# Kernel optimization log

Hardware: AMD Instinct MI355X
Metric: run time of the kernel (lower is better)

The kernel has to match this reference:

```python
import jax, jax.numpy as jnp
import numpy as np

N = 100000

def _gcn_layer(x, W, b, src, dst, norm):
    # dense transform then sparse normalized aggregation (scatter-add)
    h = x @ W                                  # [N, out]
    msg = h[src] * norm[:, None]               # [E+N, out]
    agg = jax.ops.segment_sum(msg, dst, num_segments=N)
    return agg + b


def setup_inputs() -> dict:
    key = jax.random.key(0)
    ks = jax.random.split(key, 12)
    num_features, hidden, num_classes = 128, 128, 32
    E = 3200000
    x = jax.random.normal(ks[0], (N, num_features), dtype=jnp.float32)
    edge_index = jax.random.randint(ks[1], (2, E), 0, N, dtype=jnp.int64)

    def glorot(k, fan_in, fan_out):
        s = (6.0 / (fan_in + fan_out)) ** 0.5
        return jax.random.uniform(k, (fan_in, fan_out), jnp.float32, -s, s)

    return {
        "x": x,
        "edge_index": edge_index,
        "W1": glorot(ks[2], num_features, hidden), "b1": jnp.zeros((hidden,), jnp.float32),
        "W2": glorot(ks[3], hidden, hidden),       "b2": jnp.zeros((hidden,), jnp.float32),
        "W3": glorot(ks[4], hidden, hidden),       "b3": jnp.zeros((hidden,), jnp.float32),
        "W4": glorot(ks[5], hidden, num_classes),  "b4": jnp.zeros((num_classes,), jnp.float32),
    }


def reference(x, edge_index, W1, b1, W2, b2, W3, b3, W4, b4):
    # GCNConv semantics: add self-loops, symmetric degree normalization
    loop = jnp.arange(N, dtype=edge_index.dtype)
    src = jnp.concatenate([edge_index[0], loop])   # [E+N]
    dst = jnp.concatenate([edge_index[1], loop])   # [E+N]
    deg = jax.ops.segment_sum(jnp.ones_like(dst, dtype=x.dtype), dst, num_segments=N)
    dinv = jnp.where(deg > 0, deg ** -0.5, 0.0)
    norm = dinv[src] * dinv[dst]                   # [E+N]

    h = _gcn_layer(x, W1, b1, src, dst, norm)
    h = jax.nn.relu(h)                              # dropout: eval mode -> identity
    h = _gcn_layer(h, W2, b2, src, dst, norm)
    h = jax.nn.relu(h)
    h = _gcn_layer(h, W3, b3, src, dst, norm)
    h = jax.nn.relu(h)
    h = _gcn_layer(h, W4, b4, src, dst, norm)
    return jax.nn.log_softmax(h, axis=1)
```

## Files before the change

### kernel.cpp

```cpp
#include <hip/hip_runtime.h>
#include <hip/hip_bf16.h>
#include <math.h>

#define NNODES 100000
#define NBMAX 512
#define CH 8192

typedef __hip_bfloat16 bf16;
typedef __attribute__((ext_vector_type(8))) short short8;
typedef __attribute__((ext_vector_type(4))) float f32x4;
typedef __attribute__((ext_vector_type(2))) float f32x2;

__device__ inline unsigned pack_bf16x2(float a, float b) {
    __hip_bfloat162 p;
    p.x = __float2bfloat16(a);
    p.y = __float2bfloat16(b);
    return *(unsigned*)&p;
}

__device__ inline float2 unpack_bf16x2(unsigned u) {
    __hip_bfloat162 p = *(__hip_bfloat162*)&u;
    return make_float2(__bfloat162float(p.x), __bfloat162float(p.y));
}

__device__ inline unsigned char f32_to_fp8(float v) {
    int p = __builtin_amdgcn_cvt_pk_fp8_f32(v, v, 0, false);
    return (unsigned char)(p & 0xff);
}

__global__ __launch_bounds__(256) void prep_w_all(const float* __restrict__ W1, bf16* __restrict__ wt1,
                                                  const float* __restrict__ W2, bf16* __restrict__ wt2,
                                                  const float* __restrict__ W3, bf16* __restrict__ wt3,
                                                  const float* __restrict__ W4, bf16* __restrict__ wt4,
                                                  int* __restrict__ bcount, int* __restrict__ done,
                                                  unsigned* __restrict__ zrow) {
    int b = blockIdx.x, t = threadIdx.x;
    if (b == 0) {
        for (int i = t; i < NBMAX; i += 256) bcount[i] = 0;
        if (t == 0) *done = 0;
        if (t < 32) zrow[t] = 0u;
    }
    const float* W; bf16* WT; int Nout, idx0;
    if (b < 64)       { W = W1; WT = wt1; Nout = 128; idx0 = b * 256; }
    else if (b < 128) { W = W2; WT = wt2; Nout = 128; idx0 = (b - 64) * 256; }
    else if (b < 192) { W = W3; WT = wt3; Nout = 128; idx0 = (b - 128) * 256; }
    else              { W = W4; WT = wt4; Nout = 32;  idx0 = (b - 192) * 256; }
    int idx = idx0 + t;
    if (idx < 128 * Nout) {
        int nn = idx >> 7;
        int kk = idx & 127;
        WT[idx] = __float2bfloat16(W[kk * Nout + nn]);
    }
}

__global__ __launch_bounds__(256) void bucket_hist_scan(const int* __restrict__ dst,
                                                        int* __restrict__ bcount,
                                                        int* __restrict__ boff,
                                                        int* __restrict__ bcursor,
                                                        int* __restrict__ done,
                                                        int E, int nb, int nblocks) {
    __shared__ int hist[NBMAX];
    __shared__ int ticket_s;
    __shared__ int wsum[4];
    int t = threadIdx.x;
    for (int i = t; i < NBMAX; i += 256) hist[i] = 0;
    __syncthreads();
    int e0 = blockIdx.x * CH;
#pragma unroll
    for (int k = 0; k < 32; ++k) {
        int e = e0 + t + k * 256;
        if (e < E) atomicAdd(&hist[dst[e] >> 8], 1);
    }
    __syncthreads();
    for (int i = t; i < nb; i += 256)
        if (hist[i]) atomicAdd(&bcount[i], hist[i]);
    __threadfence();
    __syncthreads();
    if (t == 0) ticket_s = atomicAdd(done, 1);
    __syncthreads();
    if (ticket_s != nblocks - 1) return;
    __threadfence();
    int i0 = t * 2, i1v = t * 2 + 1;
    int a  = (i0  < nb) ? atomicAdd(&bcount[i0], 0) : 0;
    int bb = (i1v < nb) ? atomicAdd(&bcount[i1v], 0) : 0;
    int v = a + bb;
    int lane = t & 63, wv = t >> 6;
    int incl = v;
#pragma unroll
    for (int dd = 1; dd < 64; dd <<= 1) {
        int x = __shfl_up(incl, dd, 64);
        if (lane >= dd) incl += x;
    }
    if (lane == 63) wsum[wv] = incl;
    __syncthreads();
    int wo = 0;
    for (int k = 0; k < wv; ++k) wo += wsum[k];
    int excl = wo + incl - v;
    if (i0 <= nb)  { boff[i0]  = excl;     if (i0  < nb) bcursor[i0]  = excl; }
    if (i1v <= nb) { boff[i1v] = excl + a; if (i1v < nb) bcursor[i1v] = excl + a; }
}

__global__ __launch_bounds__(256) void partition(const int* __restrict__ src,
                                                 const int* __restrict__ dst,
                                                 int* __restrict__ bcursor,
                                                 int* __restrict__ part, int E, int nb) {
    __shared__ int hist[NBMAX];
    __shared__ int cursor[NBMAX];
    int t = threadIdx.x;
    int e0 = blockIdx.x * CH;
    for (int i = t; i < NBMAX; i += 256) hist[i] = 0;
    __syncthreads();
    int mys[32], myd[32];
#pragma unroll
    for (int k = 0; k < 32; ++k) {
        int e = e0 + t + k * 256;
        int s = 0, dd = -1;
        if (e < E) { s = src[e]; dd = dst[e]; }
        mys[k] = s; myd[k] = dd;
        if (dd >= 0) atomicAdd(&hist[dd >> 8], 1);
    }
    __syncthreads();
    for (int i = t; i < nb; i += 256) {
        int c = hist[i];
        cursor[i] = c ? atomicAdd(&bcursor[i], c) : 0;
    }
    __syncthreads();
#pragma unroll
    for (int k = 0; k < 32; ++k) {
        int dd = myd[k];
        if (dd >= 0) {
            int lpos = atomicAdd(&cursor[dd >> 8], 1);
            part[lpos] = mys[k] | ((dd & 255) << 24);
        }
    }
}

__global__ __launch_bounds__(256) void nodes_fill(const int* __restrict__ part,
                                                  const int* __restrict__ boff,
                                                  float* __restrict__ dinv,
                                                  int2* __restrict__ off2,
                                                  int* __restrict__ edges, int n) {
    __shared__ int ndeg[256];
    __shared__ int ws2[4];
    __shared__ int offl[256];
    int b = blockIdx.x;
    int t = threadIdx.x;
    ndeg[t] = 0;
    __syncthreads();
    int r0 = boff[b], r1 = boff[b + 1];
    for (int i = r0 + t; i < r1; i += 256)
        atomicAdd(&ndeg[((unsigned)part[i]) >> 24], 1);
    __syncthreads();
    int deg = ndeg[t];
    int node = b * 256 + t;
    int lane = t & 63, wv = t >> 6;
    int incl = deg;
#pragma unroll
    for (int d = 1; d < 64; d <<= 1) {
        int x = __shfl_up(incl, d, 64);
        if (lane >= d) incl += x;
    }
    if (lane == 63) ws2[wv] = incl;
    __syncthreads();
    int wo = 0;
    for (int k = 0; k < wv; ++k) wo += ws2[k];
    int node_off = r0 + wo + incl - deg;
    if (node < n) {
        off2[node] = make_int2(node_off, node_off + deg);
        dinv[node] = rsqrtf((float)(deg + 1));
    }
    offl[t] = node_off;
    ndeg[t] = 0;
    __syncthreads();
    for (int i = r0 + t; i < r1; i += 256) {
        int rec = part[i];
        int dloc = ((unsigned)rec) >> 24;
        int lpos = atomicAdd(&ndeg[dloc], 1);
        edges[offl[dloc] + lpos] = rec & 0xFFFFFF;
    }
}

#define WSTRIDE 136

__global__ __launch_bounds__(256) void gemm128_f32A(const float* __restrict__ A,
                                                    const bf16* __restrict__ WT,
                                                    const float* __restrict__ dinv,
                                                    unsigned char* __restrict__ C, int n) {
    __shared__ bf16 wl[128 * WSTRIDE];
    int t = threadIdx.x;
#pragma unroll
    for (int l = 0; l < 8; ++l) {
        int chunk = t + l * 256;
        int row = chunk >> 4, ch = chunk & 15;
        *(uint4*)&wl[row * WSTRIDE + ch * 8] = *(const uint4*)&WT[row * 128 + ch * 8];
    }
    __syncthreads();
    int wave = t >> 6, lane = t & 63;
    int m = lane & 15, q = lane >> 4;
    int row_base = blockIdx.x * 128 + wave * 32;
    int r0 = min(row_base + m, n - 1);
    int r1 = min(row_base + 16 + m, n - 1);

    f32x4 acc[2][8];
#pragma unroll
    for (int g = 0; g < 2; ++g)
#pragma unroll
        for (int c = 0; c < 8; ++c) acc[g][c] = (f32x4)(0.f);

#pragma unroll
    for (int kt = 0; kt < 4; ++kt) {
        short8 af[2];
#pragma unroll
        for (int g = 0; g < 2; ++g) {
            const float* ap = &A[(size_t)(g ? r1 : r0) * 128 + kt * 32 + q * 8];
            float4 f0 = *(const float4*)ap;
            float4 f1 = *(const float4*)(ap + 4);
            union { uint4 u; short8 s; } cv;
            cv.u.x = pack_bf16x2(f0.x, f0.y);
            cv.u.y = pack_bf16x2(f0.z, f0.w);
            cv.u.z = pack_bf16x2(f1.x, f1.y);
            cv.u.w = pack_bf16x2(f1.z, f1.w);
            af[g] = cv.s;
        }
#pragma unroll
        for (int c = 0; c < 8; ++c) {
            short8 bf = *(const short8*)&wl[(c * 16 + m) * WSTRIDE + kt * 32 + q * 8];
            acc[0][c] = __builtin_amdgcn_mfma_f32_16x16x32_bf16(af[0], bf, acc[0][c], 0, 0, 0);
            acc[1][c] = __builtin_amdgcn_mfma_f32_16x16x32_bf16(af[1], bf, acc[1][c], 0, 0, 0);
        }
    }
    float dv[2][4];
#pragma unroll
    for (int g = 0; g < 2; ++g)
#pragma unroll
        for (int r = 0; r < 4; ++r) {
            int row = row_base + g * 16 + q * 4 + r;
            dv[g][r] = (row < n) ? dinv[row] : 0.f;
        }
#pragma unroll
    for (int g = 0; g < 2; ++g)
#pragma unroll
        for (int c = 0; c < 8; ++c)
#pragma unroll
            for (int r = 0; r < 4; ++r) {
                int row = row_base + g * 16 + q * 4 + r;
                if (row < n) C[(size_t)row * 128 + c * 16 + m] = f32_to_fp8(acc[g][c][r] * dv[g][r]);
            }
}

__global__ __launch_bounds__(256) void gemm128_bf16A(const bf16* __restrict__ A,
                                                     const bf16* __restrict__ WT,
                                                     const float* __restrict__ dinv,
                                                     unsigned char* __restrict__ C, int n) {
    __shared__ bf16 wl[128 * WSTRIDE];
    int t = threadIdx.x;
#pragma unroll
    for (int l = 0; l < 8; ++l) {
        int chunk = t + l * 256;
        int row = chunk >> 4, ch = chunk & 15;
        *(uint4*)&wl[row * WSTRIDE + ch * 8] = *(const uint4*)&WT[row * 128 + ch * 8];
    }
    __syncthreads();
    int wave = t >> 6, lane = t & 63;
    int m = lane & 15, q = lane >> 4;
    int row_base = blockIdx.x * 128 + wave * 32;
    int r0 = min(row_base + m, n - 1);
    int r1 = min(row_base + 16 + m, n - 1);

    f32x4 acc[2][8];
#pragma unroll
    for (int g = 0; g < 2; ++g)
#pragma unroll
        for (int c = 0; c < 8; ++c) acc[g][c] = (f32x4)(0.f);

#pragma unroll
    for (int kt = 0; kt < 4; ++kt) {
        short8 a0 = *(const short8*)&A[(size_t)r0 * 128 + kt * 32 + q * 8];
        short8 a1 = *(const short8*)&A[(size_t)r1 * 128 + kt * 32 + q * 8];
#pragma unroll
        for (int c = 0; c < 8; ++c) {
            short8 bf = *(const short8*)&wl[(c * 16 + m) * WSTRIDE + kt * 32 + q * 8];
            acc[0][c] = __builtin_amdgcn_mfma_f32_16x16x32_bf16(a0, bf, acc[0][c], 0, 0, 0);
            acc[1][c] = __builtin_amdgcn_mfma_f32_16x16x32_bf16(a1, bf, acc[1][c], 0, 0, 0);
        }
    }
    float dv[2][4];
#pragma unroll
    for (int g = 0; g < 2; ++g)
#pragma unroll
        for (int r = 0; r < 4; ++r) {
            int row = row_base + g * 16 + q * 4 + r;
            dv[g][r] = (row < n) ? dinv[row] : 0.f;
        }
#pragma unroll
    for (int g = 0; g < 2; ++g)
#pragma unroll
        for (int c = 0; c < 8; ++c)
#pragma unroll
            for (int r = 0; r < 4; ++r) {
                int row = row_base + g * 16 + q * 4 + r;
                if (row < n) C[(size_t)row * 128 + c * 16 + m] = f32_to_fp8(acc[g][c][r] * dv[g][r]);
            }
}

__global__ __launch_bounds__(256) void gemm32_bf16A(const bf16* __restrict__ A,
                                                    const bf16* __restrict__ WT,
                                                    const float* __restrict__ dinv,
                                                    bf16* __restrict__ C, int n) {
    if (blockIdx.x == 0 && threadIdx.x < 32)
        C[(size_t)n * 32 + threadIdx.x] = __float2bfloat16(0.f);
    int wave = threadIdx.x >> 6;
    int lane = threadIdx.x & 63;
    int m = lane & 15;
    int q = lane >> 4;
    int row_base = blockIdx.x * 64 + wave * 16;
    int arow = min(row_base + m, n - 1);

    f32x4 acc[2];
    acc[0] = (f32x4)(0.f);
    acc[1] = (f32x4)(0.f);

#pragma unroll
    for (int kt = 0; kt < 4; ++kt) {
        short8 af = *(const short8*)&A[(size_t)arow * 128 + kt * 32 + q * 8];
#pragma unroll
        for (int c = 0; c < 2; ++c) {
            short8 bf = *(const short8*)&WT[(size_t)(c * 16 + m) * 128 + kt * 32 + q * 8];
            acc[c] = __builtin_amdgcn_mfma_f32_16x16x32_bf16(af, bf, acc[c], 0, 0, 0);
        }
    }
    float dv[4];
#pragma unroll
    for (int r = 0; r < 4; ++r) {
        int row = row_base + q * 4 + r;
        dv[r] = (row < n) ? dinv[row] : 0.f;
    }
#pragma unroll
    for (int c = 0; c < 2; ++c)
#pragma unroll
        for (int r = 0; r < 4; ++r) {
            int row = row_base + q * 4 + r;
            if (row < n) C[(size_t)row * 32 + c * 16 + m] = __float2bfloat16(acc[c][r] * dv[r]);
        }
}

__global__ __launch_bounds__(256) void agg128(const unsigned char* __restrict__ h,
                                              const int2* __restrict__ off2,
                                              const int* __restrict__ edges,
                                              const float* __restrict__ dinv,
                                              const float* __restrict__ bias,
                                              bf16* __restrict__ out, int n) {
    int wid = (blockIdx.x * blockDim.x + threadIdx.x) >> 6;
    if (wid >= n) return;
    int lane = threadIdx.x & 63;
    int g = lane >> 3;
    int d = lane & 7;
    int l32 = lane & 31;
    const char* hb = (const char*)h;
    unsigned doff = (unsigned)(d << 4);

    int2 rng = off2[wid];
    int i0 = rng.x, i1 = rng.y;
    int deg = i1 - i0;
    int rem = deg & 31;
    int tail = i1 - rem;

    int tw = n;
    if (rem) {
        int te = edges[tail + l32];
        tw = (l32 < rem) ? te : n;
    }

    f32x2 A[8];
#pragma unroll
    for (int q = 0; q < 8; ++q) A[q] = (f32x2){0.f, 0.f};

    if (g == 0) {
        uint4 su = *(const uint4*)(hb + (((unsigned)wid << 7) | doff));
        A[0] += __builtin_amdgcn_cvt_pk_f32_fp8((int)su.x, false);
        A[1] += __builtin_amdgcn_cvt_pk_f32_fp8((int)su.x, true);
        A[2] += __builtin_amdgcn_cvt_pk_f32_fp8((int)su.y, false);
        A[3] += __builtin_amdgcn_cvt_pk_f32_fp8((int)su.y, true);
        A[4] += __builtin_amdgcn_cvt_pk_f32_fp8((int)su.z, false);
        A[5] += __builtin_amdgcn_cvt_pk_f32_fp8((int)su.z, true);
        A[6] += __builtin_amdgcn_cvt_pk_f32_fp8((int)su.w, false);
        A[7] += __builtin_amdgcn_cvt_pk_f32_fp8((int)su.w, true);
    }

    int i = i0;
    int ew;
    if (i + 32 <= i1) ew = edges[i + l32];
    while (i + 32 <= i1) {
        int idxs[4];
#pragma unroll
        for (int j = 0; j < 4; ++j) idxs[j] = __shfl(ew, j * 8 + g, 64);
        uint4 uu[4];
#pragma unroll
        for (int j = 0; j < 4; ++j)
            uu[j] = *(const uint4*)(hb + (((unsigned)idxs[j] << 7) | doff));
        int inext = i + 32;
        if (inext + 32 <= i1) ew = edges[inext + l32];
#pragma unroll
        for (int j = 0; j < 4; ++j) {
            A[0] += __builtin_amdgcn_cvt_pk_f32_fp8((int)uu[j].x, false);
            A[1] += __builtin_amdgcn_cvt_pk_f32_fp8((int)uu[j].x, true);
            A[2] += __builtin_amdgcn_cvt_pk_f32_fp8((int)uu[j].y, false);
            A[3] += __builtin_amdgcn_cvt_pk_f32_fp8((int)uu[j].y, true);
            A[4] += __builtin_amdgcn_cvt_pk_f32_fp8((int)uu[j].z, false);
            A[5] += __builtin_amdgcn_cvt_pk_f32_fp8((int)uu[j].z, true);
            A[6] += __builtin_amdgcn_cvt_pk_f32_fp8((int)uu[j].w, false);
            A[7] += __builtin_amdgcn_cvt_pk_f32_fp8((int)uu[j].w, true);
        }
        i = inext;
    }
    if (rem) {
        int njg = (rem + 7) >> 3;
        int idxs[4];
        uint4 uu[4];
#pragma unroll
        for (int j = 0; j < 4; ++j)
            if (j < njg) idxs[j] = __shfl(tw, j * 8 + g, 64);
#pragma unroll
        for (int j = 0; j < 4; ++j)
            if (j < njg) uu[j] = *(const uint4*)(hb + (((unsigned)idxs[j] << 7) | doff));
#pragma unroll
        for (int j = 0; j < 4; ++j) {
            if (j < njg) {
                A[0] += __builtin_amdgcn_cvt_pk_f32_fp8((int)uu[j].x, false);
                A[1] += __builtin_amdgcn_cvt_pk_f32_fp8((int)uu[j].x, true);
                A[2] += __builtin_amdgcn_cvt_pk_f32_fp8((int)uu[j].y, false);
                A[3] += __builtin_amdgcn_cvt_pk_f32_fp8((int)uu[j].y, true);
                A[4] += __builtin_amdgcn_cvt_pk_f32_fp8((int)uu[j].z, false);
                A[5] += __builtin_amdgcn_cvt_pk_f32_fp8((int)uu[j].z, true);
                A[6] += __builtin_amdgcn_cvt_pk_f32_fp8((int)uu[j].w, false);
                A[7] += __builtin_amdgcn_cvt_pk_f32_fp8((int)uu[j].w, true);
            }
        }
    }
    bool k0 = (g & 1) != 0, k1 = (g & 2) != 0, k2 = (g & 4) != 0;
    f32x2 B1[4];
#pragma unroll
    for (int q = 0; q < 4; ++q) {
        f32x2 K = k0 ? A[q + 4] : A[q];
        f32x2 S = k0 ? A[q] : A[q + 4];
        f32x2 R; R[0] = __shfl_xor(S[0], 8, 64); R[1] = __shfl_xor(S[1], 8, 64);
        B1[q] = K + R;
    }
    f32x2 B2[2];
#pragma unroll
    for (int q = 0; q < 2; ++q) {
        f32x2 K = k1 ? B1[q + 2] : B1[q];
        f32x2 S = k1 ? B1[q] : B1[q + 2];
        f32x2 R; R[0] = __shfl_xor(S[0], 16, 64); R[1] = __shfl_xor(S[1], 16, 64);
        B2[q] = K + R;
    }
    f32x2 K3 = k2 ? B2[1] : B2[0];
    f32x2 S3 = k2 ? B2[0] : B2[1];
    f32x2 R3; R3[0] = __shfl_xor(S3[0], 32, 64); R3[1] = __shfl_xor(S3[1], 32, 64);
    f32x2 F = K3 + R3;

    int od = d * 8 + (k0 ? 4 : 0) + (k1 ? 2 : 0) + (k2 ? 1 : 0);
    float dl = dinv[wid];
    float2 bv = *(const float2*)&bias[od * 2];
    float a0 = fmaxf(F[0] * dl + bv.x, 0.f);
    float a1 = fmaxf(F[1] * dl + bv.y, 0.f);
    ((unsigned*)out)[(size_t)wid * 64 + od] = pack_bf16x2(a0, a1);
}

__global__ __launch_bounds__(256) void agg32_lsm(const bf16* __restrict__ h,
                                                 const int2* __restrict__ off2,
                                                 const int* __restrict__ edges,
                                                 const float* __restrict__ dinv,
                                                 const float* __restrict__ bias,
                                                 float* __restrict__ out, int n) {
    int idx = blockIdx.x * blockDim.x + threadIdx.x;
    int node = idx >> 5;
    if (node >= n) return;
    int lane = threadIdx.x & 63;
    int halfbase = lane & 32;
    int lane5 = lane & 31;
    int g = lane5 >> 3;
    int d = lane5 & 7;
    int l16 = lane5 & 15;
    const char* hb = (const char*)h;
    unsigned doff = (unsigned)(d << 3);

    int2 rng = off2[node];
    int i0 = rng.x, i1 = rng.y;
    int deg = i1 - i0;
    int rem = deg & 15;
    int tail = i1 - rem;

    int tw = n;
    if (rem) {
        int te = edges[tail + l16];
        tw = (l16 < rem) ? te : n;
    }

    f32x2 acc0 = {0.f, 0.f}, acc1 = {0.f, 0.f};
    {
        uint2 su = *(const uint2*)(hb + (((unsigned)node << 6) | doff));
        if (g) { su.x = 0u; su.y = 0u; }
        float2 f0 = unpack_bf16x2(su.x), f1 = unpack_bf16x2(su.y);
        acc0[0] += f0.x; acc0[1] += f0.y; acc1[0] += f1.x; acc1[1] += f1.y;
    }
    int i = i0;
    int ew;
    if (i + 16 <= i1) ew = edges[i + l16];
    while (i + 16 <= i1) {
        int idxs[4];
#pragma unroll
        for (int j = 0; j < 4; ++j) idxs[j] = __shfl(ew, halfbase + j * 4 + g, 64);
        uint2 uu[4];
#pragma unroll
        for (int j = 0; j < 4; ++j)
            uu[j] = *(const uint2*)(hb + (((unsigned)idxs[j] << 6) | doff));
        int inext = i + 16;
        if (inext + 16 <= i1) ew = edges[inext + l16];
#pragma unroll
        for (int j = 0; j < 4; ++j) {
            float2 f0 = unpack_bf16x2(uu[j].x), f1 = unpack_bf16x2(uu[j].y);
            acc0[0] += f0.x; acc0[1] += f0.y; acc1[0] += f1.x; acc1[1] += f1.y;
        }
        i = inext;
    }
    if (rem) {
        int njg = (rem + 3) >> 2;
        int idxs[4];
        uint2 uu[4];
#pragma unroll
        for (int j = 0; j < 4; ++j)
            if (j < njg) idxs[j] = __shfl(tw, halfbase + j * 4 + g, 64);
#pragma unroll
        for (int j = 0; j < 4; ++j)
            if (j < njg) uu[j] = *(const uint2*)(hb + (((unsigned)idxs[j] << 6) | doff));
#pragma unroll
        for (int j = 0; j < 4; ++j) {
            if (j < njg) {
                float2 f0 = unpack_bf16x2(uu[j].x), f1 = unpack_bf16x2(uu[j].y);
                acc0[0] += f0.x; acc0[1] += f0.y; acc1[0] += f1.x; acc1[1] += f1.y;
            }
        }
    }
    float s0 = acc0[0], s1 = acc0[1], s2 = acc1[0], s3 = acc1[1];
    s0 += __shfl_xor(s0, 8);  s1 += __shfl_xor(s1, 8);
    s2 += __shfl_xor(s2, 8);  s3 += __shfl_xor(s3, 8);
    s0 += __shfl_xor(s0, 16); s1 += __shfl_xor(s1, 16);
    s2 += __shfl_xor(s2, 16); s3 += __shfl_xor(s3, 16);

    float dl = dinv[node];
    float4 bv = *(const float4*)&bias[d * 4];
    float a0 = s0 * dl + bv.x;
    float a1 = s1 * dl + bv.y;
    float a2 = s2 * dl + bv.z;
    float a3 = s3 * dl + bv.w;
    float m = fmaxf(fmaxf(a0, a1), fmaxf(a2, a3));
    for (int dd = 1; dd < 8; dd <<= 1) m = fmaxf(m, __shfl_xor(m, dd));
    float e = expf(a0 - m) + expf(a1 - m) + expf(a2 - m) + expf(a3 - m);
    for (int dd = 1; dd < 8; dd <<= 1) e += __shfl_xor(e, dd);
    float lse = m + logf(e);
    if (g == 0)
        *(float4*)&out[(size_t)node * 32 + d * 4] =
            make_float4(a0 - lse, a1 - lse, a2 - lse, a3 - lse);
}

extern "C" void kernel_launch(void* const* d_in, const int* in_sizes, int n_in,
                              void* d_out, int out_size, void* d_ws, size_t ws_size,
                              hipStream_t stream) {
    const float* x  = (const float*)d_in[0];
    const int*   ei = (const int*)d_in[1];
    const float* W1 = (const float*)d_in[2];
    const float* b1 = (const float*)d_in[3];
    const float* W2 = (const float*)d_in[4];
    const float* b2 = (const float*)d_in[5];
    const float* W3 = (const float*)d_in[6];
    const float* b3 = (const float*)d_in[7];
    const float* W4 = (const float*)d_in[8];
    const float* b4 = (const float*)d_in[9];
    float* out = (float*)d_out;

    const int N = NNODES;
    const int E = in_sizes[1] / 2;
    const int nb = (N + 255) / 256;

    char* ws = (char*)d_ws;
    size_t o = 0;
    auto alloc = [&](size_t bytes) -> void* {
        void* p = ws + o;
        o += (bytes + 255) & ~(size_t)255;
        return p;
    };
    int*   bcount  = (int*)alloc((size_t)NBMAX * 4);
    int*   boff    = (int*)alloc((size_t)(NBMAX + 1) * 4);
    int*   bcursor = (int*)alloc((size_t)NBMAX * 4);
    int*   done    = (int*)alloc(4);
    int2*  off2    = (int2*)alloc((size_t)N * 8);
    float* dinv    = (float*)alloc((size_t)N * 4);
    int*   part    = (int*)alloc((size_t)E * 8);
    int*   edges   = (int*)alloc((size_t)(E + 64) * 4);
    bf16*  wt1     = (bf16*)alloc((size_t)128 * 128 * 2);
    bf16*  wt2     = (bf16*)alloc((size_t)128 * 128 * 2);
    bf16*  wt3     = (bf16*)alloc((size_t)128 * 128 * 2);
    bf16*  wt4     = (bf16*)alloc((size_t)32 * 128 * 2);
    unsigned char* hbuf = (unsigned char*)alloc((size_t)(N + 1) * 128);
    bf16*  gbuf    = (bf16*)part;

    const int* srcv = ei;
    const int* dstv = ei + E;

    int pblocks = (E + CH - 1) / CH;

    prep_w_all<<<208, 256, 0, stream>>>(W1, wt1, W2, wt2, W3, wt3, W4, wt4,
                                        bcount, done, (unsigned*)(hbuf + (size_t)N * 128));
    bucket_hist_scan<<<pblocks, 256, 0, stream>>>(dstv, bcount, boff, bcursor, done,
                                                  E, nb, pblocks);
    partition<<<pblocks, 256, 0, stream>>>(srcv, dstv, bcursor, part, E, nb);
    nodes_fill<<<nb, 256, 0, stream>>>(part, boff, dinv, off2, edges, N);

    int gemm128_blocks = (N + 127) / 128;
    int gemm32_blocks = (N + 63) / 64;
    int agg128_blocks = (N + 3) / 4;
    int agg32_blocks = (N * 32 + 255) / 256;

    gemm128_f32A<<<gemm128_blocks, 256, 0, stream>>>(x, wt1, dinv, hbuf, N);
    agg128<<<agg128_blocks, 256, 0, stream>>>(hbuf, off2, edges, dinv, b1, gbuf, N);
    gemm128_bf16A<<<gemm128_blocks, 256, 0, stream>>>(gbuf, wt2, dinv, hbuf, N);
    agg128<<<agg128_blocks, 256, 0, stream>>>(hbuf, off2, edges, dinv, b2, gbuf, N);
    gemm128_bf16A<<<gemm128_blocks, 256, 0, stream>>>(gbuf, wt3, dinv, hbuf, N);
    agg128<<<agg128_blocks, 256, 0, stream>>>(hbuf, off2, edges, dinv, b3, gbuf, N);
    gemm32_bf16A<<<gemm32_blocks, 256, 0, stream>>>(gbuf, wt4, dinv, (bf16*)hbuf, N);
    agg32_lsm<<<agg32_blocks, 256, 0, stream>>>((const bf16*)hbuf, off2, edges, dinv, b4, out, N);
}
```

Baseline: 471.4 us.

## Add fixed-width padded neighbor table so aggregation avoids CSR loop for low degree

Builds a per-node padded array of up to 64 source indices (filled with the zero-row sentinel) plus a packed degree/dinv record, and rewrites both aggregation kernels to load all neighbors in one unrolled batch without data-dependent loops, falling back to CSR only for degree above 64. This removes the dependent offset->edges load chain and loop overhead per node. It costs an extra 25.6 MB fill in prep and extra scattered writes in nodes_fill, and padded lanes do wasted loads of the sentinel row.

```diff
diff --git a/kernel.cpp b/kernel.cpp
--- a/kernel.cpp
+++ b/kernel.cpp
@@ -33,13 +33,18 @@
                                                   const float* __restrict__ W3, bf16* __restrict__ wt3,
                                                   const float* __restrict__ W4, bf16* __restrict__ wt4,
                                                   int* __restrict__ bcount, int* __restrict__ done,
-                                                  unsigned* __restrict__ zrow) {
+                                                  unsigned* __restrict__ zrow,
+                                                  int4* __restrict__ ef4, int n) {
     int b = blockIdx.x, t = threadIdx.x;
     if (b == 0) {
         for (int i = t; i < NBMAX; i += 256) bcount[i] = 0;
         if (t == 0) *done = 0;
         if (t < 32) zrow[t] = 0u;
     }
+    int tot4 = n * 16;
+    int4 fill = make_int4(n, n, n, n);
+    for (int i = b * 256 + t; i < tot4; i += 208 * 256) ef4[i] = fill;
+
     const float* W; bf16* WT; int Nout, idx0;
     if (b < 64)       { W = W1; WT = wt1; Nout = 128; idx0 = b * 256; }
     else if (b < 128) { W = W2; WT = wt2; Nout = 128; idx0 = (b - 64) * 256; }
@@ -139,7 +144,9 @@
                                                   const int* __restrict__ boff,
                                                   float* __restrict__ dinv,
                                                   int2* __restrict__ off2,
-                                                  int* __restrict__ edges, int n) {
+                                                  int2* __restrict__ degdinv,
+                                                  int* __restrict__ edges,
+                                                  int* __restrict__ ef, int n) {
     __shared__ int ndeg[256];
     __shared__ int ws2[4];
     __shared__ int offl[256];
@@ -166,8 +173,10 @@
     for (int k = 0; k < wv; ++k) wo += ws2[k];
     int node_off = r0 + wo + incl - deg;
     if (node < n) {
+        float rq = rsqrtf((float)(deg + 1));
         off2[node] = make_int2(node_off, node_off + deg);
-        dinv[node] = rsqrtf((float)(deg + 1));
+        dinv[node] = rq;
+        degdinv[node] = make_int2(deg, __float_as_int(rq));
     }
     offl[t] = node_off;
     ndeg[t] = 0;
@@ -176,7 +185,10 @@
         int rec = part[i];
         int dloc = ((unsigned)rec) >> 24;
         int lpos = atomicAdd(&ndeg[dloc], 1);
-        edges[offl[dloc] + lpos] = rec & 0xFFFFFF;
+        int sv = rec & 0xFFFFFF;
+        edges[offl[dloc] + lpos] = sv;
+        if (lpos < 64)
+            ef[(((size_t)b << 8) + dloc) * 64 + lpos] = sv;
     }
 }
 
@@ -345,9 +357,10 @@
 }
 
 __global__ __launch_bounds__(256) void agg128(const unsigned char* __restrict__ h,
+                                              const int2* __restrict__ degdinv,
                                               const int2* __restrict__ off2,
                                               const int* __restrict__ edges,
-                                              const float* __restrict__ dinv,
+                                              const int* __restrict__ ef,
                                               const float* __restrict__ bias,
                                               bf16* __restrict__ out, int n) {
     int wid = (blockIdx.x * blockDim.x + threadIdx.x) >> 6;
@@ -355,28 +368,20 @@
     int lane = threadIdx.x & 63;
     int g = lane >> 3;
     int d = lane & 7;
-    int l32 = lane & 31;
     const char* hb = (const char*)h;
     unsigned doff = (unsigned)(d << 4);
 
-    int2 rng = off2[wid];
-    int i0 = rng.x, i1 = rng.y;
-    int deg = i1 - i0;
-    int rem = deg & 31;
-    int tail = i1 - rem;
-
-    int tw = n;
-    if (rem) {
-        int te = edges[tail + l32];
-        tw = (l32 < rem) ? te : n;
-    }
+    int2 dd = degdinv[wid];
+    int w = ef[(size_t)wid * 64 + lane];
+    uint4 su = *(const uint4*)(hb + (((unsigned)wid << 7) | doff));
+
+    int deg = dd.x;
+    float dl = __int_as_float(dd.y);
 
     f32x2 A[8];
 #pragma unroll
     for (int q = 0; q < 8; ++q) A[q] = (f32x2){0.f, 0.f};
-
     if (g == 0) {
-        uint4 su = *(const uint4*)(hb + (((unsigned)wid << 7) | doff));
         A[0] += __builtin_amdgcn_cvt_pk_f32_fp8((int)su.x, false);
         A[1] += __builtin_amdgcn_cvt_pk_f32_fp8((int)su.x, true);
         A[2] += __builtin_amdgcn_cvt_pk_f32_fp8((int)su.y, false);
@@ -387,45 +392,19 @@
         A[7] += __builtin_amdgcn_cvt_pk_f32_fp8((int)su.w, true);
     }
 
-    int i = i0;
-    int ew;
-    if (i + 32 <= i1) ew = edges[i + l32];
-    while (i + 32 <= i1) {
-        int idxs[4];
-#pragma unroll
-        for (int j = 0; j < 4; ++j) idxs[j] = __shfl(ew, j * 8 + g, 64);
-        uint4 uu[4];
-#pragma unroll
-        for (int j = 0; j < 4; ++j)
-            uu[j] = *(const uint4*)(hb + (((unsigned)idxs[j] << 7) | doff));
-        int inext = i + 32;
-        if (inext + 32 <= i1) ew = edges[inext + l32];
-#pragma unroll
-        for (int j = 0; j < 4; ++j) {
-            A[0] += __builtin_amdgcn_cvt_pk_f32_fp8((int)uu[j].x, false);
-            A[1] += __builtin_amdgcn_cvt_pk_f32_fp8((int)uu[j].x, true);
-            A[2] += __builtin_amdgcn_cvt_pk_f32_fp8((int)uu[j].y, false);
-            A[3] += __builtin_amdgcn_cvt_pk_f32_fp8((int)uu[j].y, true);
-            A[4] += __builtin_amdgcn_cvt_pk_f32_fp8((int)uu[j].z, false);
-            A[5] += __builtin_amdgcn_cvt_pk_f32_fp8((int)uu[j].z, true);
-            A[6] += __builtin_amdgcn_cvt_pk_f32_fp8((int)uu[j].w, false);
-            A[7] += __builtin_amdgcn_cvt_pk_f32_fp8((int)uu[j].w, true);
-        }
-        i = inext;
-    }
-    if (rem) {
-        int njg = (rem + 7) >> 3;
-        int idxs[4];
-        uint4 uu[4];
-#pragma unroll
-        for (int j = 0; j < 4; ++j)
-            if (j < njg) idxs[j] = __shfl(tw, j * 8 + g, 64);
-#pragma unroll
-        for (int j = 0; j < 4; ++j)
-            if (j < njg) uu[j] = *(const uint4*)(hb + (((unsigned)idxs[j] << 7) | doff));
-#pragma unroll
-        for (int j = 0; j < 4; ++j) {
-            if (j < njg) {
+    int nj = min((deg + 7) >> 3, 8);
+    {
+        int idxs[8];
+        uint4 uu[8];
+#pragma unroll
+        for (int j = 0; j < 8; ++j)
+            if (j < nj) idxs[j] = __shfl(w, j * 8 + g, 64);
+#pragma unroll
+        for (int j = 0; j < 8; ++j)
+            if (j < nj) uu[j] = *(const uint4*)(hb + (((unsigned)idxs[j] << 7) | doff));
+#pragma unroll
+        for (int j = 0; j < 8; ++j) {
+            if (j < nj) {
                 A[0] += __builtin_amdgcn_cvt_pk_f32_fp8((int)uu[j].x, false);
                 A[1] += __builtin_amdgcn_cvt_pk_f32_fp8((int)uu[j].x, true);
                 A[2] += __builtin_amdgcn_cvt_pk_f32_fp8((int)uu[j].y, false);
@@ -437,6 +416,39 @@
             }
         }
     }
+    if (deg > 64) {
+        int2 r = off2[wid];
+        int i = r.x + 64, i1 = r.y;
+        int l32 = lane & 31;
+        while (i < i1) {
+            int rem = i1 - i;
+            int e = i + l32;
+            int wv = (l32 < rem) ? edges[e] : n;
+            int njg = min((rem + 7) >> 3, 4);
+            int idxs[4];
+            uint4 uu[4];
+#pragma unroll
+            for (int j = 0; j < 4; ++j)
+                if (j < njg) idxs[j] = __shfl(wv, j * 8 + g, 64);
+#pragma unroll
+            for (int j = 0; j < 4; ++j)
+                if (j < njg) uu[j] = *(const uint4*)(hb + (((unsigned)idxs[j] << 7) | doff));
+#pragma unroll
+            for (int j = 0; j < 4; ++j) {
+                if (j < njg) {
+                    A[0] += __builtin_amdgcn_cvt_pk_f32_fp8((int)uu[j].x, false);
+                    A[1] += __builtin_amdgcn_cvt_pk_f32_fp8((int)uu[j].x, true);
+                    A[2] += __builtin_amdgcn_cvt_pk_f32_fp8((int)uu[j].y, false);
+                    A[3] += __builtin_amdgcn_cvt_pk_f32_fp8((int)uu[j].y, true);
+                    A[4] += __builtin_amdgcn_cvt_pk_f32_fp8((int)uu[j].z, false);
+                    A[5] += __builtin_amdgcn_cvt_pk_f32_fp8((int)uu[j].z, true);
+                    A[6] += __builtin_amdgcn_cvt_pk_f32_fp8((int)uu[j].w, false);
+                    A[7] += __builtin_amdgcn_cvt_pk_f32_fp8((int)uu[j].w, true);
+                }
+            }
+            i += 32;
+        }
+    }
     bool k0 = (g & 1) != 0, k1 = (g & 2) != 0, k2 = (g & 4) != 0;
     f32x2 B1[4];
 #pragma unroll
@@ -460,7 +472,6 @@
     f32x2 F = K3 + R3;
 
     int od = d * 8 + (k0 ? 4 : 0) + (k1 ? 2 : 0) + (k2 ? 1 : 0);
-    float dl = dinv[wid];
     float2 bv = *(const float2*)&bias[od * 2];
     float a0 = fmaxf(F[0] * dl + bv.x, 0.f);
     float a1 = fmaxf(F[1] * dl + bv.y, 0.f);
@@ -468,9 +479,10 @@
 }
 
 __global__ __launch_bounds__(256) void agg32_lsm(const bf16* __restrict__ h,
+                                                 const int2* __restrict__ degdinv,
                                                  const int2* __restrict__ off2,
                                                  const int* __restrict__ edges,
-                                                 const float* __restrict__ dinv,
+                                                 const int* __restrict__ ef,
                                                  const float* __restrict__ bias,
                                                  float* __restrict__ out, int n) {
     int idx = blockIdx.x * blockDim.x + threadIdx.x;
@@ -481,65 +493,82 @@
     int lane5 = lane & 31;
     int g = lane5 >> 3;
     int d = lane5 & 7;
-    int l16 = lane5 & 15;
     const char* hb = (const char*)h;
     unsigned doff = (unsigned)(d << 3);
 
-    int2 rng = off2[node];
-    int i0 = rng.x, i1 = rng.y;
-    int deg = i1 - i0;
-    int rem = deg & 15;
-    int tail = i1 - rem;
-
-    int tw = n;
-    if (rem) {
-        int te = edges[tail + l16];
-        tw = (l16 < rem) ? te : n;
-    }
+    int2 dd = degdinv[node];
+    int wlo = ef[(size_t)node * 64 + lane5];
+    int whi = ef[(size_t)node * 64 + 32 + lane5];
+    uint2 su = *(const uint2*)(hb + (((unsigned)node << 6) | doff));
+
+    int deg = dd.x;
+    float dl = __int_as_float(dd.y);
 
     f32x2 acc0 = {0.f, 0.f}, acc1 = {0.f, 0.f};
-    {
-        uint2 su = *(const uint2*)(hb + (((unsigned)node << 6) | doff));
-        if (g) { su.x = 0u; su.y = 0u; }
+    if (g == 0) {
         float2 f0 = unpack_bf16x2(su.x), f1 = unpack_bf16x2(su.y);
         acc0[0] += f0.x; acc0[1] += f0.y; acc1[0] += f1.x; acc1[1] += f1.y;
     }
-    int i = i0;
-    int ew;
-    if (i + 16 <= i1) ew = edges[i + l16];
-    while (i + 16 <= i1) {
-        int idxs[4];
-#pragma unroll
-        for (int j = 0; j < 4; ++j) idxs[j] = __shfl(ew, halfbase + j * 4 + g, 64);
-        uint2 uu[4];
-#pragma unroll
-        for (int j = 0; j < 4; ++j)
-            uu[j] = *(const uint2*)(hb + (((unsigned)idxs[j] << 6) | doff));
-        int inext = i + 16;
-        if (inext + 16 <= i1) ew = edges[inext + l16];
-#pragma unroll
-        for (int j = 0; j < 4; ++j) {
-            float2 f0 = unpack_bf16x2(uu[j].x), f1 = unpack_bf16x2(uu[j].y);
-            acc0[0] += f0.x; acc0[1] += f0.y; acc1[0] += f1.x; acc1[1] += f1.y;
-        }
-        i = inext;
-    }
-    if (rem) {
-        int njg = (rem + 3) >> 2;
-        int idxs[4];
-        uint2 uu[4];
-#pragma unroll
-        for (int j = 0; j < 4; ++j)
-            if (j < njg) idxs[j] = __shfl(tw, halfbase + j * 4 + g, 64);
-#pragma unroll
-        for (int j = 0; j < 4; ++j)
-            if (j < njg) uu[j] = *(const uint2*)(hb + (((unsigned)idxs[j] << 6) | doff));
-#pragma unroll
-        for (int j = 0; j < 4; ++j) {
-            if (j < njg) {
+    int nj = min((deg + 3) >> 2, 16);
+    {
+        int idxs[8];
+        uint2 uu[8];
+#pragma unroll
+        for (int j = 0; j < 8; ++j)
+            if (j < nj) idxs[j] = __shfl(wlo, halfbase + j * 4 + g, 64);
+#pragma unroll
+        for (int j = 0; j < 8; ++j)
+            if (j < nj) uu[j] = *(const uint2*)(hb + (((unsigned)idxs[j] << 6) | doff));
+#pragma unroll
+        for (int j = 0; j < 8; ++j) {
+            if (j < nj) {
                 float2 f0 = unpack_bf16x2(uu[j].x), f1 = unpack_bf16x2(uu[j].y);
                 acc0[0] += f0.x; acc0[1] += f0.y; acc1[0] += f1.x; acc1[1] += f1.y;
             }
+        }
+    }
+    if (nj > 8) {
+        int idxs[8];
+        uint2 uu[8];
+#pragma unroll
+        for (int j = 0; j < 8; ++j)
+            if (j + 8 < nj) idxs[j] = __shfl(whi, halfbase + j * 4 + g, 64);
+#pragma unroll
+        for (int j = 0; j < 8; ++j)
+            if (j + 8 < nj) uu[j] = *(const uint2*)(hb + (((unsigned)idxs[j] << 6) | doff));
+#pragma unroll
+        for (int j = 0; j < 8; ++j) {
+            if (j + 8 < nj) {
+                float2 f0 = unpack_bf16x2(uu[j].x), f1 = unpack_bf16x2(uu[j].y);
+                acc0[0] += f0.x; acc0[1] += f0.y; acc1[0] += f1.x; acc1[1] += f1.y;
+            }
+        }
+    }
+    if (deg > 64) {
+        int2 r = off2[node];
+        int i = r.x + 64, i1 = r.y;
+        int l16 = lane5 & 15;
+        while (i < i1) {
+            int rem = i1 - i;
+            int e = i + l16;
+            int wv = (l16 < rem) ? edges[e] : n;
+            int njg = min((rem + 3) >> 2, 4);
+            int idxs[4];
+            uint2 uu[4];
+#pragma unroll
+            for (int j = 0; j < 4; ++j)
+                if (j < njg) idxs[j] = __shfl(wv, halfbase + j * 4 + g, 64);
+#pragma unroll
+            for (int j = 0; j < 4; ++j)
+                if (j < njg) uu[j] = *(const uint2*)(hb + (((unsigned)idxs[j] << 6) | doff));
+#pragma unroll
+            for (int j = 0; j < 4; ++j) {
+                if (j < njg) {
+                    float2 f0 = unpack_bf16x2(uu[j].x), f1 = unpack_bf16x2(uu[j].y);
+                    acc0[0] += f0.x; acc0[1] += f0.y; acc1[0] += f1.x; acc1[1] += f1.y;
+                }
+            }
+            i += 16;
         }
     }
     float s0 = acc0[0], s1 = acc0[1], s2 = acc1[0], s3 = acc1[1];
@@ -548,16 +577,15 @@
     s0 += __shfl_xor(s0, 16); s1 += __shfl_xor(s1, 16);
     s2 += __shfl_xor(s2, 16); s3 += __shfl_xor(s3, 16);
 
-    float dl = dinv[node];
     float4 bv = *(const float4*)&bias[d * 4];
     float a0 = s0 * dl + bv.x;
     float a1 = s1 * dl + bv.y;
     float a2 = s2 * dl + bv.z;
     float a3 = s3 * dl + bv.w;
     float m = fmaxf(fmaxf(a0, a1), fmaxf(a2, a3));
-    for (int dd = 1; dd < 8; dd <<= 1) m = fmaxf(m, __shfl_xor(m, dd));
+    for (int dd2 = 1; dd2 < 8; dd2 <<= 1) m = fmaxf(m, __shfl_xor(m, dd2));
     float e = expf(a0 - m) + expf(a1 - m) + expf(a2 - m) + expf(a3 - m);
-    for (int dd = 1; dd < 8; dd <<= 1) e += __shfl_xor(e, dd);
+    for (int dd2 = 1; dd2 < 8; dd2 <<= 1) e += __shfl_xor(e, dd2);
     float lse = m + logf(e);
     if (g == 0)
         *(float4*)&out[(size_t)node * 32 + d * 4] =
@@ -595,9 +623,11 @@
     int*   bcursor = (int*)alloc((size_t)NBMAX * 4);
     int*   done    = (int*)alloc(4);
     int2*  off2    = (int2*)alloc((size_t)N * 8);
+    int2*  degdinv = (int2*)alloc((size_t)N * 8);
     float* dinv    = (float*)alloc((size_t)N * 4);
     int*   part    = (int*)alloc((size_t)E * 8);
     int*   edges   = (int*)alloc((size_t)(E + 64) * 4);
+    int*   ef      = (int*)alloc((size_t)N * 64 * 4);
     bf16*  wt1     = (bf16*)alloc((size_t)128 * 128 * 2);
     bf16*  wt2     = (bf16*)alloc((size_t)128 * 128 * 2);
     bf16*  wt3     = (bf16*)alloc((size_t)128 * 128 * 2);
@@ -611,11 +641,12 @@
     int pblocks = (E + CH - 1) / CH;
 
     prep_w_all<<<208, 256, 0, stream>>>(W1, wt1, W2, wt2, W3, wt3, W4, wt4,
-                                        bcount, done, (unsigned*)(hbuf + (size_t)N * 128));
+                                        bcount, done, (unsigned*)(hbuf + (size_t)N * 128),
+                                        (int4*)ef, N);
     bucket_hist_scan<<<pblocks, 256, 0, stream>>>(dstv, bcount, boff, bcursor, done,
                                                   E, nb, pblocks);
     partition<<<pblocks, 256, 0, stream>>>(srcv, dstv, bcursor, part, E, nb);
-    nodes_fill<<<nb, 256, 0, stream>>>(part, boff, dinv, off2, edges, N);
+    nodes_fill<<<nb, 256, 0, stream>>>(part, boff, dinv, off2, degdinv, edges, ef, N);
 
     int gemm128_blocks = (N + 127) / 128;
     int gemm32_blocks = (N + 63) / 64;
@@ -623,11 +654,11 @@
     int agg32_blocks = (N * 32 + 255) / 256;
 
     gemm128_f32A<<<gemm128_blocks, 256, 0, stream>>>(x, wt1, dinv, hbuf, N);
-    agg128<<<agg128_blocks, 256, 0, stream>>>(hbuf, off2, edges, dinv, b1, gbuf, N);
+    agg128<<<agg128_blocks, 256, 0, stream>>>(hbuf, degdinv, off2, edges, ef, b1, gbuf, N);
     gemm128_bf16A<<<gemm128_blocks, 256, 0, stream>>>(gbuf, wt2, dinv, hbuf, N);
-    agg128<<<agg128_blocks, 256, 0, stream>>>(hbuf, off2, edges, dinv, b2, gbuf, N);
+    agg128<<<agg128_blocks, 256, 0, stream>>>(hbuf, degdinv, off2, edges, ef, b2, gbuf, N);
     gemm128_bf16A<<<gemm128_blocks, 256, 0, stream>>>(gbuf, wt3, dinv, hbuf, N);
-    agg128<<<agg128_blocks, 256, 0, stream>>>(hbuf, off2, edges, dinv, b3, gbuf, N);
+    agg128<<<agg128_blocks, 256, 0, stream>>>(hbuf, degdinv, off2, edges, ef, b3, gbuf, N);
     gemm32_bf16A<<<gemm32_blocks, 256, 0, stream>>>(gbuf, wt4, dinv, (bf16*)hbuf, N);
-    agg32_lsm<<<agg32_blocks, 256, 0, stream>>>((const bf16*)hbuf, off2, edges, dinv, b4, out, N);
-}
+    agg32_lsm<<<agg32_blocks, 256, 0, stream>>>((const bf16*)hbuf, degdinv, off2, edges, ef, b4, out, N);
+}
```

Measured after the change: 538.0 us. 1.14x slower.
